# Optimization experiments

Measured on AMD Instinct MI355X. Metric: run time of the kernel, lower is better.

## Reference

```python
import jax, jax.numpy as jnp
import numpy as np

TEMPERATURE = 1.0          # max(args.matching_temperature=1.0, 1e-6)
CONSISTENCY_WEIGHT = 0.5   # max(args.matching_consistency_weight=0.5, 0.0)
EPS = 1e-6

N, M, D, K = 16384, 16384, 128, 5


def setup_inputs() -> dict:
    key = jax.random.key(0)
    k1, k2, k3 = jax.random.split(key, 3)
    query = jax.random.normal(k1, (N, D), dtype=jnp.float32)
    memory_bank = jax.random.normal(k2, (M, D), dtype=jnp.float32)
    # per-memory-entry neighbor scale (positive), as in _build_patch_library_statistics
    neighbor_scale_bank = jax.random.uniform(k3, (M,), dtype=jnp.float32) + 0.1
    return {"query": query, "memory_bank": memory_bank,
            "neighbor_scale_bank": neighbor_scale_bank, "k": K}


def reference(query, memory_bank, neighbor_scale_bank, k):
    # Euclidean cdist: [N, M]
    q2 = jnp.sum(query * query, axis=-1, keepdims=True)            # [N,1]
    m2 = jnp.sum(memory_bank * memory_bank, axis=-1)               # [M]
    d2 = q2 + m2 - 2.0 * (query @ memory_bank.T)                   # [N,M]
    dist = jnp.sqrt(jnp.maximum(d2, 1e-12))

    # torch.topk(largest=False) -> k smallest distances, ascending
    neg_d, knn_indices = jax.lax.top_k(-dist, k)                   # [N,k]
    knn_distances = -neg_d

    # adaptive_knn reduction (_reduce_knn_distances)
    weights = jax.nn.softmax(-knn_distances / TEMPERATURE, axis=1)
    weighted_distance = jnp.sum(weights * knn_distances, axis=1)   # [N]

    neighbor_scale = jnp.mean(neighbor_scale_bank[knn_indices], axis=1)  # [N]
    normalized_distance = weighted_distance / jnp.maximum(neighbor_scale, EPS)

    mean_d = jnp.mean(knn_distances, axis=1)
    std_d = jnp.sqrt(jnp.maximum(
        jnp.mean((knn_distances - mean_d[:, None]) ** 2, axis=1), 0.0))  # unbiased=False
    consistency = std_d / jnp.maximum(mean_d, EPS)

    return normalized_distance * (1.0 + CONSISTENCY_WEIGHT * consistency)
```

## Files before the change

kernel.cpp:

```cpp
#include <hip/hip_runtime.h>
#include <hip/hip_bf16.h>
#include <math.h>

#define N_Q 16384
#define N_M 16384
#define DIM 128
#define KNN 5
#define SPLITS 8
#define COLS_PER_SPLIT (N_M / SPLITS)
#define ITERS (COLS_PER_SPLIT / 128)
#define BROWS 256
#define TSEL 8
#define TSEL2 16
#define LLIST 4
#define BIGF 3.0e38f

typedef __bf16 bf16x8 __attribute__((ext_vector_type(8)));
typedef float f32x4 __attribute__((ext_vector_type(4)));

__device__ __forceinline__ void gl2lds16(const void* g, void* l) {
    __builtin_amdgcn_global_load_lds(
        (const __attribute__((address_space(1))) void*)g,
        (__attribute__((address_space(3))) void*)l, 16, 0, 0);
}

__device__ __forceinline__ unsigned umed3(unsigned a, unsigned b, unsigned c) {
    unsigned d;
    asm("v_med3_u32 %0, %1, %2, %3" : "=v"(d) : "v"(a), "v"(b), "v"(c));
    return d;
}

template <int D>
__device__ __forceinline__ void insD(unsigned (&L)[D], unsigned k) {
#pragma unroll
    for (int i = D - 1; i >= 1; --i) L[i] = umed3(L[i - 1], L[i], k);
    L[0] = min(L[0], k);
}

__global__ void prep_kernel(const float* __restrict__ q,
                            const float* __restrict__ mem,
                            float* __restrict__ q2, float* __restrict__ m2,
                            float* __restrict__ m2b,
                            __hip_bfloat16* __restrict__ qb,
                            __hip_bfloat16* __restrict__ mb) {
    int gt = blockIdx.x * blockDim.x + threadIdx.x;
    int wid = gt >> 6;
    int lane = gt & 63;
    bool isq = wid < N_Q;
    int r = isq ? wid : wid - N_Q;
    const float* src = (isq ? q : mem) + (size_t)r * DIM;
    __hip_bfloat16* bdst = (isq ? qb : mb) + (size_t)r * DIM;
    float2 v = reinterpret_cast<const float2*>(src)[lane];
    float sc = isq ? 1.0f : -2.0f;
    __hip_bfloat162 bv;
    bv.x = __float2bfloat16(sc * v.x);
    bv.y = __float2bfloat16(sc * v.y);
    reinterpret_cast<__hip_bfloat162*>(bdst)[lane] = bv;
    float s = fmaf(v.x, v.x, v.y * v.y);
#pragma unroll
    for (int off = 32; off > 0; off >>= 1) s += __shfl_down(s, off, 64);
    if (lane == 0) {
        if (isq) {
            q2[r] = s;
        } else {
            m2[r] = s;
            m2b[r] = s + 256.0f;
        }
    }
}

__global__ __launch_bounds__(256, 2) void knn_tops_kernel(
    const __hip_bfloat16* __restrict__ qb, const __hip_bfloat16* __restrict__ mb,
    const float* __restrict__ m2b, unsigned* __restrict__ candK) {
    __shared__ __align__(16) unsigned char smem[65536];
    const int tid = threadIdx.x;
    const int w = tid >> 6;
    const int lane = tid & 63;
    const int i16 = lane & 15;
    const int g = lane >> 4;
    const int row0 = blockIdx.x * BROWS;
    const int col0 = blockIdx.y * COLS_PER_SPLIT;

    bf16x8 afrag[4][4];
#pragma unroll
    for (int ti = 0; ti < 4; ++ti) {
        const __hip_bfloat16* qrow =
            qb + (size_t)(row0 + w * 64 + ti * 16 + i16) * DIM;
#pragma unroll
        for (int ks = 0; ks < 4; ++ks)
            afrag[ti][ks] = *reinterpret_cast<const bf16x8*>(qrow + ks * 32 + g * 8);
    }

    unsigned lst[16][LLIST];
#pragma unroll
    for (int rr = 0; rr < 16; ++rr)
#pragma unroll
        for (int j = 0; j < LLIST; ++j) lst[rr][j] = 0xFFFFFFFFu;

    const int lds_base = i16 * 256 + ((g ^ (i16 & 7)) << 4);
    int soff[8];
#pragma unroll
    for (int it = 0; it < 8; ++it) {
        int fg = w * 512 + it * 64 + lane;
        int c = fg >> 4, sg = fg & 15;
        int gk = (sg & 8) | ((sg ^ c) & 7);
        soff[it] = c * DIM + gk * 8;
    }
    const __hip_bfloat16* mbt = mb + (size_t)col0 * DIM;

#pragma unroll
    for (int it = 0; it < 8; ++it)
        gl2lds16(mbt + soff[it], smem + w * 8192 + it * 1024);
    mbt += 128 * DIM;
    __syncthreads();

    for (int t = 0; t < ITERS; ++t) {
        unsigned char* cbuf = smem + ((t & 1) << 15);
        if (t + 1 < ITERS) {
            unsigned char* nbuf = smem + (((t + 1) & 1) << 15);
#pragma unroll
            for (int it = 0; it < 8; ++it)
                gl2lds16(mbt + soff[it], nbuf + w * 8192 + it * 1024);
            mbt += 128 * DIM;
        }

        float m2r[8];
        unsigned colv[8];
#pragma unroll
        for (int h = 0; h < 2; ++h)
#pragma unroll
            for (int c = 0; c < 4; ++c) {
                int cl = col0 + t * 128 + h * 64 + c * 16 + i16;
                m2r[h * 4 + c] = m2b[cl];
                colv[h * 4 + c] = (unsigned)cl;
            }
#pragma unroll
        for (int half = 0; half < 2; ++half) {
#pragma unroll
            for (int cc = 0; cc < 2; ++cc) {
                f32x4 acc[4][2];
#pragma unroll
                for (int ti = 0; ti < 4; ++ti)
#pragma unroll
                    for (int c2 = 0; c2 < 2; ++c2) {
                        float m = m2r[half * 4 + cc * 2 + c2];
                        acc[ti][c2] = (f32x4){m, m, m, m};
                    }
#pragma unroll
                for (int ks = 0; ks < 4; ++ks) {
                    const unsigned char* bp =
                        cbuf + (lds_base ^ (ks << 6)) + half * 16384;
#pragma unroll
                    for (int c2 = 0; c2 < 2; ++c2) {
                        int ct = cc * 2 + c2;
                        bf16x8 bfr =
                            *reinterpret_cast<const bf16x8*>(bp + ct * 4096);
#pragma unroll
                        for (int ti = 0; ti < 4; ++ti)
                            acc[ti][c2] = __builtin_amdgcn_mfma_f32_16x16x32_bf16(
                                afrag[ti][ks], bfr, acc[ti][c2], 0, 0, 0);
                    }
                }
#pragma unroll
                for (int ti = 0; ti < 4; ++ti) {
#pragma unroll
                    for (int r = 0; r < 4; ++r) {
                        const int rr = ti * 4 + r;
#pragma unroll
                        for (int c2 = 0; c2 < 2; ++c2) {
                            unsigned k = (__float_as_uint(acc[ti][c2][r]) &
                                          0xFFFFC000u) |
                                         colv[half * 4 + cc * 2 + c2];
                            insD(lst[rr], k);
                        }
                    }
                }
            }
        }
        __syncthreads();
    }


#pragma unroll
    for (int rr = 0; rr < 16; ++rr) {
        unsigned pv[LLIST];
#pragma unroll
        for (int j = 0; j < LLIST; ++j)
            pv[j] = (unsigned)__shfl_xor((int)lst[rr][j], 8, 64);
#pragma unroll
        for (int j = 0; j < LLIST; ++j) insD(lst[rr], pv[j]);
    }
    unsigned* MG = (unsigned*)smem;
    if (i16 < 8) {
#pragma unroll
        for (int rr = 0; rr < 16; ++rr) {
            int row = w * 64 + (rr >> 2) * 16 + g * 4 + (rr & 3);
#pragma unroll
            for (int j = 0; j < LLIST; ++j)
                MG[row * 33 + i16 * LLIST + j] = lst[rr][j];
        }
    }
    __syncthreads();
    {
        unsigned bk[TSEL];
#pragma unroll
        for (int j = 0; j < TSEL; ++j) bk[j] = 0xFFFFFFFFu;
        for (int c = 0; c < 32; ++c) {
            unsigned k = MG[tid * 33 + c];
            insD(bk, k);
        }
        size_t base = (size_t)(row0 + tid) * (SPLITS * TSEL) + blockIdx.y * TSEL;
        *reinterpret_cast<uint4*>(candK + base) =
            make_uint4(bk[0], bk[1], bk[2], bk[3]);
        *reinterpret_cast<uint4*>(candK + base + 4) =
            make_uint4(bk[4], bk[5], bk[6], bk[7]);
    }
}

__global__ void merge_kernel(const unsigned* __restrict__ candK,
                             int* __restrict__ candI2) {
    int row = blockIdx.x * blockDim.x + threadIdx.x;
    const unsigned* ck = candK + (size_t)row * (SPLITS * TSEL);
    unsigned v[TSEL2];
#pragma unroll
    for (int j = 0; j < TSEL2; ++j) v[j] = 0xFFFFFFFFu;
    for (int s4 = 0; s4 < 16; ++s4) {
        uint4 kk = reinterpret_cast<const uint4*>(ck)[s4];
        insD(v, kk.x);
        insD(v, kk.y);
        insD(v, kk.z);
        insD(v, kk.w);
    }
#pragma unroll
    for (int j = 0; j < TSEL2; ++j)
        candI2[(size_t)row * TSEL2 + j] = (int)(v[j] & 0x3FFFu);
}

__global__ __launch_bounds__(256) void finalize_kernel(
    const float* __restrict__ q, const float* __restrict__ mem,
    const float* __restrict__ q2, const float* __restrict__ m2,
    const int* __restrict__ candI2, const float* __restrict__ scaleb,
    float* __restrict__ out) {
    int wv = threadIdx.x >> 6, lane = threadIdx.x & 63;
    int n = blockIdx.x * 4 + wv;
    int cand = lane >> 2, qd = lane & 3;
    int ci = candI2[(size_t)n * TSEL2 + cand];
    const float4* qr = reinterpret_cast<const float4*>(q + (size_t)n * DIM) + qd * 8;
    const float4* mr = reinterpret_cast<const float4*>(mem + (size_t)ci * DIM) + qd * 8;
    float dot = 0.f;
#pragma unroll
    for (int k = 0; k < 8; ++k) {
        float4 a = qr[k], b = mr[k];
        dot = fmaf(a.x, b.x, fmaf(a.y, b.y, fmaf(a.z, b.z, fmaf(a.w, b.w, dot))));
    }
    dot += __shfl_xor(dot, 1, 64);
    dot += __shfl_xor(dot, 2, 64);
    float v = (qd == 0) ? (q2[n] + m2[ci] - 2.f * dot) : BIGF;

    float dk[KNN]; int ik[KNN];
#pragma unroll
    for (int r = 0; r < KNN; ++r) {
        float mv = v; int ml = lane;
#pragma unroll
        for (int off = 32; off > 0; off >>= 1) {
            float ov = __shfl_xor(mv, off, 64);
            int   ol = __shfl_xor(ml, off, 64);
            if (ov < mv || (ov == mv && ol < ml)) { mv = ov; ml = ol; }
        }
        dk[r] = sqrtf(fmaxf(mv, 1e-12f));
        ik[r] = __shfl(ci, ml, 64);
        if (lane == ml) v = BIGF;
    }
    if (lane == 0) {
        float dmin = dk[0];
        float se = 0.f, wd = 0.f, sm = 0.f, ssc = 0.f;
#pragma unroll
        for (int j = 0; j < KNN; ++j) {
            float e = expf(-(dk[j] - dmin));
            se += e;
            wd = fmaf(e, dk[j], wd);
            sm += dk[j];
            ssc += scaleb[ik[j]];
        }
        wd /= se;
        float scale = ssc * 0.2f;
        float nd = wd / fmaxf(scale, 1e-6f);
        float mean = sm * 0.2f;
        float var = 0.f;
#pragma unroll
        for (int j = 0; j < KNN; ++j) {
            float dd = dk[j] - mean;
            var = fmaf(dd, dd, var);
        }
        var *= 0.2f;
        float cons = sqrtf(var) / fmaxf(mean, 1e-6f);
        out[n] = nd * (1.f + 0.5f * cons);
    }
}

extern "C" void kernel_launch(void* const* d_in, const int* in_sizes, int n_in,
                              void* d_out, int out_size, void* d_ws,
                              size_t ws_size, hipStream_t stream) {
    const float* query  = (const float*)d_in[0];
    const float* mem    = (const float*)d_in[1];
    const float* scaleb = (const float*)d_in[2];
    float* out = (float*)d_out;

    float* q2 = (float*)d_ws;
    float* m2 = q2 + N_Q;
    float* m2b = m2 + N_M;
    __hip_bfloat16* qb = (__hip_bfloat16*)(m2b + N_M);
    __hip_bfloat16* mb = qb + (size_t)N_Q * DIM;
    unsigned* candK = (unsigned*)(mb + (size_t)N_M * DIM);
    int* candI2 = (int*)(candK + (size_t)N_Q * SPLITS * TSEL);

    prep_kernel<<<(N_Q + N_M) / 4, 256, 0, stream>>>(query, mem, q2, m2, m2b,
                                                     qb, mb);
    dim3 gridB(N_Q / BROWS, SPLITS);
    knn_tops_kernel<<<gridB, 256, 0, stream>>>(qb, mb, m2b, candK);
    merge_kernel<<<N_Q / 256, 256, 0, stream>>>(candK, candI2);
    finalize_kernel<<<N_Q / 4, 256, 0, stream>>>(query, mem, q2, m2, candI2,
                                                 scaleb, out);
}
```

Measured before the change: 191.3 us.

## Software-pipeline MFMA chunks with top-k selection using ping-pong accumulators

Restructures the inner loop so the MFMA work for one column chunk is issued before the top-k insertion for the previous chunk. Two accumulator sets alternate, and the last chunk of each tile is carried into the next iteration. The aim is to let matrix-core work overlap with the scalar/VALU selection work. In exchange it needs more accumulator registers, which could raise register pressure and spill under the launch bounds (256, 2). The initial BIGF accumulator keeps the first, dummy selection harmless.

```diff
diff --git a/kernel.cpp b/kernel.cpp
--- a/kernel.cpp
+++ b/kernel.cpp
@@ -69,6 +69,47 @@
     }
 }
 
+__device__ __forceinline__ void mfma_chunk(const unsigned char* cbuf,
+                                           int lds_base,
+                                           const bf16x8 (&afrag)[4][4],
+                                           const float (&m2r)[8], int c,
+                                           f32x4 (&acc)[4][2]) {
+#pragma unroll
+    for (int ti = 0; ti < 4; ++ti)
+#pragma unroll
+        for (int c2 = 0; c2 < 2; ++c2) {
+            float m = m2r[c * 2 + c2];
+            acc[ti][c2] = (f32x4){m, m, m, m};
+        }
+#pragma unroll
+    for (int ks = 0; ks < 4; ++ks) {
+        const unsigned char* bp =
+            cbuf + (lds_base ^ (ks << 6)) + (c >> 1) * 16384;
+#pragma unroll
+        for (int c2 = 0; c2 < 2; ++c2) {
+            bf16x8 bfr = *reinterpret_cast<const bf16x8*>(
+                bp + ((c & 1) * 2 + c2) * 4096);
+#pragma unroll
+            for (int ti = 0; ti < 4; ++ti)
+                acc[ti][c2] = __builtin_amdgcn_mfma_f32_16x16x32_bf16(
+                    afrag[ti][ks], bfr, acc[ti][c2], 0, 0, 0);
+        }
+    }
+}
+
+__device__ __forceinline__ void select_chunk(unsigned (&lst)[16][LLIST],
+                                             const f32x4 (&acc)[4][2],
+                                             unsigned cv0, unsigned cv1) {
+#pragma unroll
+    for (int ti = 0; ti < 4; ++ti)
+#pragma unroll
+        for (int r = 0; r < 4; ++r) {
+            const int rr = ti * 4 + r;
+            insD(lst[rr], (__float_as_uint(acc[ti][0][r]) & 0xFFFFC000u) | cv0);
+            insD(lst[rr], (__float_as_uint(acc[ti][1][r]) & 0xFFFFC000u) | cv1);
+        }
+}
+
 __global__ __launch_bounds__(256, 2) void knn_tops_kernel(
     const __hip_bfloat16* __restrict__ qb, const __hip_bfloat16* __restrict__ mb,
     const float* __restrict__ m2b, unsigned* __restrict__ candK) {
@@ -108,14 +149,22 @@
     }
     const __hip_bfloat16* mbt = mb + (size_t)col0 * DIM;
 
+    f32x4 accA[4][2], accB[4][2];
+#pragma unroll
+    for (int ti = 0; ti < 4; ++ti)
+#pragma unroll
+        for (int c2 = 0; c2 < 2; ++c2)
+            accB[ti][c2] = (f32x4){BIGF, BIGF, BIGF, BIGF};
+    unsigned pcv0 = 0, pcv1 = 0;
+
 #pragma unroll
     for (int it = 0; it < 8; ++it)
         gl2lds16(mbt + soff[it], smem + w * 8192 + it * 1024);
     mbt += 128 * DIM;
-    __syncthreads();
 
     for (int t = 0; t < ITERS; ++t) {
-        unsigned char* cbuf = smem + ((t & 1) << 15);
+        __syncthreads();
+        const unsigned char* cbuf = smem + ((t & 1) << 15);
         if (t + 1 < ITERS) {
             unsigned char* nbuf = smem + (((t + 1) & 1) << 15);
 #pragma unroll
@@ -127,59 +176,26 @@
         float m2r[8];
         unsigned colv[8];
 #pragma unroll
-        for (int h = 0; h < 2; ++h)
-#pragma unroll
-            for (int c = 0; c < 4; ++c) {
-                int cl = col0 + t * 128 + h * 64 + c * 16 + i16;
-                m2r[h * 4 + c] = m2b[cl];
-                colv[h * 4 + c] = (unsigned)cl;
-            }
-#pragma unroll
-        for (int half = 0; half < 2; ++half) {
-#pragma unroll
-            for (int cc = 0; cc < 2; ++cc) {
-                f32x4 acc[4][2];
-#pragma unroll
-                for (int ti = 0; ti < 4; ++ti)
-#pragma unroll
-                    for (int c2 = 0; c2 < 2; ++c2) {
-                        float m = m2r[half * 4 + cc * 2 + c2];
-                        acc[ti][c2] = (f32x4){m, m, m, m};
-                    }
-#pragma unroll
-                for (int ks = 0; ks < 4; ++ks) {
-                    const unsigned char* bp =
-                        cbuf + (lds_base ^ (ks << 6)) + half * 16384;
-#pragma unroll
-                    for (int c2 = 0; c2 < 2; ++c2) {
-                        int ct = cc * 2 + c2;
-                        bf16x8 bfr =
-                            *reinterpret_cast<const bf16x8*>(bp + ct * 4096);
-#pragma unroll
-                        for (int ti = 0; ti < 4; ++ti)
-                            acc[ti][c2] = __builtin_amdgcn_mfma_f32_16x16x32_bf16(
-                                afrag[ti][ks], bfr, acc[ti][c2], 0, 0, 0);
-                    }
-                }
-#pragma unroll
-                for (int ti = 0; ti < 4; ++ti) {
-#pragma unroll
-                    for (int r = 0; r < 4; ++r) {
-                        const int rr = ti * 4 + r;
-#pragma unroll
-                        for (int c2 = 0; c2 < 2; ++c2) {
-                            unsigned k = (__float_as_uint(acc[ti][c2][r]) &
-                                          0xFFFFC000u) |
-                                         colv[half * 4 + cc * 2 + c2];
-                            insD(lst[rr], k);
-                        }
-                    }
-                }
-            }
-        }
-        __syncthreads();
-    }
-
+        for (int cg = 0; cg < 8; ++cg) {
+            int cl = col0 + t * 128 + cg * 16 + i16;
+            m2r[cg] = m2b[cl];
+            colv[cg] = (unsigned)cl;
+        }
+
+        mfma_chunk(cbuf, lds_base, afrag, m2r, 0, accA);
+        select_chunk(lst, accB, pcv0, pcv1);
+        mfma_chunk(cbuf, lds_base, afrag, m2r, 1, accB);
+        select_chunk(lst, accA, colv[0], colv[1]);
+        mfma_chunk(cbuf, lds_base, afrag, m2r, 2, accA);
+        select_chunk(lst, accB, colv[2], colv[3]);
+        mfma_chunk(cbuf, lds_base, afrag, m2r, 3, accB);
+        select_chunk(lst, accA, colv[4], colv[5]);
+        pcv0 = colv[6];
+        pcv1 = colv[7];
+    }
+    select_chunk(lst, accB, pcv0, pcv1);
+
+    __syncthreads();
 
 #pragma unroll
     for (int rr = 0; rr < 16; ++rr) {
```

Measured after the change: 192.2 us. About the same (+0.4%).
